# Optimization experiments

Measured on AMD Instinct MI355X. Metric: run time of the kernel, lower is better.

## Reference

```python
import jax, jax.numpy as jnp
import numpy as np

E, NH, NL, NP = 256, 8, 4, 4
D = E // NH
SPATIAL_SHAPES = np.array([[100, 134], [50, 67], [25, 34], [13, 17]], dtype=np.int64)
B = 2


def setup_inputs() -> dict:
    key = jax.random.key(0)
    ks = jax.random.split(key, 12)
    Lin = int((SPATIAL_SHAPES[:, 0] * SPATIAL_SHAPES[:, 1]).sum())
    Lq = Lin
    s = 0.02
    return {
        'query': jax.random.normal(ks[0], (Lq, B, E), jnp.float32),
        'value': jax.random.normal(ks[1], (Lin, B, E), jnp.float32),
        'reference_points': jax.random.uniform(ks[2], (B, Lq, NL, 2), jnp.float32),
        'spatial_shapes': SPATIAL_SHAPES,
        'W_value': jax.random.normal(ks[3], (E, E), jnp.float32) * s,
        'b_value': jnp.zeros((E,), jnp.float32),
        'W_offset': jax.random.normal(ks[4], (E, NH * NL * NP * 2), jnp.float32) * s,
        'b_offset': jax.random.normal(ks[5], (NH * NL * NP * 2,), jnp.float32) * 0.5,
        'W_attn': jax.random.normal(ks[6], (E, NH * NL * NP), jnp.float32) * s,
        'b_attn': jnp.zeros((NH * NL * NP,), jnp.float32),
        'W_out': jax.random.normal(ks[7], (E, E), jnp.float32) * s,
        'b_out': jnp.zeros((E,), jnp.float32),
    }


def _ms_deform_attn(value, spatial_shapes, sampling_locations, attention_weights):
    # value: (B, Lin, NH, D); sampling_locations: (B, Lq, NH, NL, NP, 2) in [0,1]
    # attention_weights: (B, Lq, NH, NL, NP)
    b, _, nh, d = value.shape
    lq = sampling_locations.shape[1]
    npnt = sampling_locations.shape[4]
    shapes = np.asarray(spatial_shapes)
    out = jnp.zeros((b, nh, lq, d), value.dtype)
    start = 0
    for l in range(shapes.shape[0]):
        H, W = int(shapes[l, 0]), int(shapes[l, 1])
        vl = value[:, start:start + H * W].transpose(0, 2, 1, 3)  # (B, NH, H*W, D)
        loc = sampling_locations[:, :, :, l].transpose(0, 2, 1, 3, 4)  # (B, NH, Lq, P, 2)
        # grid_sample align_corners=False convention (matches CUDA kernel)
        x = loc[..., 0] * W - 0.5
        y = loc[..., 1] * H - 0.5
        x0 = jnp.floor(x)
        y0 = jnp.floor(y)
        dx = x - x0
        dy = y - y0
        x0i = x0.astype(jnp.int32)
        y0i = y0.astype(jnp.int32)
        acc = jnp.zeros((b, nh, lq, npnt, d), value.dtype)
        corners = [
            (x0i, y0i, (1.0 - dx) * (1.0 - dy)),
            (x0i + 1, y0i, dx * (1.0 - dy)),
            (x0i, y0i + 1, (1.0 - dx) * dy),
            (x0i + 1, y0i + 1, dx * dy),
        ]
        for xi, yi, w in corners:
            valid = ((xi >= 0) & (xi < W) & (yi >= 0) & (yi < H)).astype(value.dtype)
            idx = jnp.clip(yi, 0, W - 1 if False else H - 1) * 0  # placeholder removed below
            idx = jnp.clip(yi, 0, H - 1) * W + jnp.clip(xi, 0, W - 1)  # (B, NH, Lq, P)
            g = jnp.take_along_axis(vl, idx.reshape(b, nh, -1)[..., None], axis=2)
            g = g.reshape(b, nh, lq, npnt, d)
            acc = acc + g * (w * valid)[..., None]
        awl = attention_weights[:, :, :, l].transpose(0, 2, 1, 3)  # (B, NH, Lq, P)
        out = out + jnp.einsum('bhqpd,bhqp->bhqd', acc, awl)
        start += H * W
    return out.transpose(0, 2, 1, 3).reshape(b, lq, nh * d)  # (B, Lq, E)


def reference(query, value, reference_points, spatial_shapes,
              W_value, b_value, W_offset, b_offset, W_attn, b_attn, W_out, b_out):
    q = query.transpose(1, 0, 2)   # (B, Lq, E)
    v = value.transpose(1, 0, 2)   # (B, Lin, E)
    b, lq, _ = q.shape
    lin = v.shape[1]
    v = (v @ W_value + b_value).reshape(b, lin, NH, D)
    offsets = (q @ W_offset + b_offset).reshape(b, lq, NH, NL, NP, 2)
    attn = (q @ W_attn + b_attn).reshape(b, lq, NH, NL, NP)
    attn = jax.nn.softmax(attn, axis=-1)  # softmax over points (as in source)
    shapes_f = jnp.asarray(np.asarray(spatial_shapes), jnp.float32)
    offset_normalizer = jnp.stack([shapes_f[:, 1], shapes_f[:, 0]], -1)  # (NL, 2) = (w, h)
    loc = reference_points[:, :, None, :, None, :] + offsets / offset_normalizer[None, None, None, :, None, :]
    out = _ms_deform_attn(v, spatial_shapes, loc, attn)  # (B, Lq, E)
    out = out @ W_out + b_out
    return out.transpose(1, 0, 2)  # (Lq, B, E)
```

## Files before the change

kernel.cpp:

```cpp
#include <hip/hip_runtime.h>
#include <math.h>

#define LQ    17821
#define MROWS 35642
#define KD    256

typedef __attribute__((ext_vector_type(8))) short bf16x8;
typedef __attribute__((ext_vector_type(4))) float f32x4;

__device__ __forceinline__ short f2bf(float f) {
  union { float f; unsigned u; } c; c.f = f;
  unsigned u = c.u;
  return (short)((u + 0x7fffu + ((u >> 16) & 1u)) >> 16);
}
__device__ __forceinline__ float bf2f(short s) {
  union { unsigned u; float f; } c;
  c.u = ((unsigned)(unsigned short)s) << 16;
  return c.f;
}

__global__ __launch_bounds__(256) void cvt_bf16(
    const float* __restrict__ src, short* __restrict__ dst, int n)
{
  int i = (blockIdx.x * 256 + threadIdx.x) * 4;
  if (i < n) {
    float4 v = *(const float4*)(src + i);
    short4 o;
    o.x = f2bf(v.x); o.y = f2bf(v.y); o.z = f2bf(v.z); o.w = f2bf(v.w);
    *(short4*)(dst + i) = o;
  }
}

__global__ __launch_bounds__(256) void wtrans_all(
    const float* __restrict__ Wv, const float* __restrict__ Woff,
    const float* __restrict__ Wat, const float* __restrict__ Wout,
    short* __restrict__ wT)
{
  int sel = blockIdx.y;
  const float* W = sel == 0 ? Wv : sel == 1 ? Woff : sel == 2 ? Wat : Wout;
  short* Wt = wT + (sel == 0 ? 0 : sel == 1 ? 65536 : sel == 2 ? 131072 : 163840);
  int N = (sel == 2) ? 128 : 256;
  int idx = blockIdx.x * 256 + threadIdx.x;
  if (idx < N * 256) {
    int n = idx >> 8, k = idx & 255;
    Wt[idx] = f2bf(W[k * N + n]);
  }
}

template<bool OUT_BF16>
__global__ __launch_bounds__(256) void gemm_bf16(
    const short* __restrict__ A, const short* __restrict__ Bt,
    const float* __restrict__ bias, void* __restrict__ Cout,
    int M, int N)
{
  __shared__ short As[128 * 40];
  __shared__ short Bs[128 * 40];

  const int tid = threadIdx.x;
  const int bm = blockIdx.x * 128;
  const int bn = blockIdx.y * 128;
  const int wave = tid >> 6;
  const int lane = tid & 63;
  const int wm = (wave & 1) * 64;
  const int wn = (wave >> 1) * 64;
  const int ln = lane & 15;
  const int lk = (lane >> 4) * 8;

  f32x4 acc[4][4];
#pragma unroll
  for (int i = 0; i < 4; ++i)
#pragma unroll
    for (int j = 0; j < 4; ++j) acc[i][j] = (f32x4){0.f, 0.f, 0.f, 0.f};

  const int r0 = tid >> 2,         s0 = (tid & 3) * 8;
  const int r1 = (tid + 256) >> 2, s1 = ((tid + 256) & 3) * 8;
  const size_t arow0 = (size_t)min(bm + r0, M - 1) * KD;
  const size_t arow1 = (size_t)min(bm + r1, M - 1) * KD;
  const size_t brow0 = (size_t)(bn + r0) * KD;
  const size_t brow1 = (size_t)(bn + r1) * KD;

  for (int k0 = 0; k0 < KD; k0 += 32) {
    bf16x8 a0 = *(const bf16x8*)(A + arow0 + k0 + s0);
    bf16x8 a1 = *(const bf16x8*)(A + arow1 + k0 + s1);
    bf16x8 b0 = *(const bf16x8*)(Bt + brow0 + k0 + s0);
    bf16x8 b1 = *(const bf16x8*)(Bt + brow1 + k0 + s1);
    __syncthreads();
    *(bf16x8*)&As[r0 * 40 + s0] = a0;
    *(bf16x8*)&As[r1 * 40 + s1] = a1;
    *(bf16x8*)&Bs[r0 * 40 + s0] = b0;
    *(bf16x8*)&Bs[r1 * 40 + s1] = b1;
    __syncthreads();

    bf16x8 af[4], bfr[4];
#pragma unroll
    for (int i = 0; i < 4; ++i)
      af[i] = *(const bf16x8*)&As[(wm + i * 16 + ln) * 40 + lk];
#pragma unroll
    for (int j = 0; j < 4; ++j)
      bfr[j] = *(const bf16x8*)&Bs[(wn + j * 16 + ln) * 40 + lk];
#pragma unroll
    for (int i = 0; i < 4; ++i)
#pragma unroll
      for (int j = 0; j < 4; ++j)
        acc[i][j] = __builtin_amdgcn_mfma_f32_16x16x32_bf16(af[i], bfr[j], acc[i][j], 0, 0, 0);
  }

#pragma unroll
  for (int j = 0; j < 4; ++j) {
    const int col = bn + wn + j * 16 + ln;
    const float bb = bias[col];
#pragma unroll
    for (int i = 0; i < 4; ++i) {
      const int row0 = bm + wm + i * 16 + (lane >> 4) * 4;
#pragma unroll
      for (int r = 0; r < 4; ++r) {
        const int row = row0 + r;
        if (row < M) {
          float v = acc[i][j][r] + bb;
          if (OUT_BF16)
            ((short*)Cout)[(size_t)row * N + col] = f2bf(v);
          else
            ((float*)Cout)[(size_t)row * N + col] = v;
        }
      }
    }
  }
}

__global__ __launch_bounds__(256) void msda_sample(
    const short* __restrict__ vproj, const float* __restrict__ offs,
    const float* __restrict__ attn, const float* __restrict__ refp,
    short* __restrict__ out)
{
  static constexpr int LVL_H[4] = {100, 50, 25, 13};
  static constexpr int LVL_W[4] = {134, 67, 34, 17};
  static constexpr int LVL_S[4] = {0, 13400, 16750, 17600};

  __shared__ int4   s_off[4 * 8 * 17];
  __shared__ float4 s_w[4 * 8 * 17];

  const int tid = threadIdx.x;
  const int m0 = blockIdx.x * 4;

#pragma unroll
  for (int it = 0; it < 2; ++it) {
    int w = tid + it * 256;
    int mr = w >> 7;
    int rest = w & 127;
    int h = rest >> 4;
    int lp = rest & 15;
    int l = lp >> 2;
    int p = lp & 3;
    int m = m0 + mr;
    if (m < MROWS) {
      int b = m & 1, q = m >> 1;
      const int Hl = LVL_H[l], Wl = LVL_W[l], Sl = LVL_S[l];
      const float fW = (float)Wl, fH = (float)Hl;

      const float* aRow = attn + (size_t)m * 128 + h * 16 + l * 4;
      float a0 = aRow[0], a1 = aRow[1], a2 = aRow[2], a3 = aRow[3];
      float mx = fmaxf(fmaxf(a0, a1), fmaxf(a2, a3));
      a0 = __expf(a0 - mx); a1 = __expf(a1 - mx);
      a2 = __expf(a2 - mx); a3 = __expf(a3 - mx);
      float sel = (p == 0) ? a0 : (p == 1) ? a1 : (p == 2) ? a2 : a3;
      float aw = sel / (a0 + a1 + a2 + a3);

      const float* oPtr = offs + (size_t)m * 256 + h * 32 + l * 8 + p * 2;
      float ox = oPtr[0], oy = oPtr[1];
      const float* rPtr = refp + ((size_t)b * LQ + q) * 8 + l * 2;
      float rx = rPtr[0], ry = rPtr[1];

      float x = (rx + ox / fW) * fW - 0.5f;
      float y = (ry + oy / fH) * fH - 0.5f;
      float x0f = floorf(x), y0f = floorf(y);
      float dx = x - x0f, dy = y - y0f;
      int x0 = (int)x0f, y0 = (int)y0f;
      int x1 = x0 + 1, y1 = y0 + 1;

      float w00 = (1.f - dx) * (1.f - dy) * aw;
      float w10 = dx * (1.f - dy) * aw;
      float w01 = (1.f - dx) * dy * aw;
      float w11 = dx * dy * aw;

      bool vx0 = (x0 >= 0) & (x0 < Wl);
      bool vx1 = (x1 >= 0) & (x1 < Wl);
      bool vy0 = (y0 >= 0) & (y0 < Hl);
      bool vy1 = (y1 >= 0) & (y1 < Hl);
      int cx0 = min(max(x0, 0), Wl - 1);
      int cx1 = min(max(x1, 0), Wl - 1);
      int cy0 = min(max(y0, 0), Hl - 1);
      int cy1 = min(max(y1, 0), Hl - 1);

      int r0 = Sl + cy0 * Wl;
      int r1 = Sl + cy1 * Wl;
      int e = (mr * 8 + h) * 17 + lp;
      s_off[e] = make_int4(((r0 + cx0) * 2 + b) << 8,
                           ((r0 + cx1) * 2 + b) << 8,
                           ((r1 + cx0) * 2 + b) << 8,
                           ((r1 + cx1) * 2 + b) << 8);
      s_w[e] = make_float4((vy0 & vx0) ? w00 : 0.f,
                           (vy0 & vx1) ? w10 : 0.f,
                           (vy1 & vx0) ? w01 : 0.f,
                           (vy1 & vx1) ? w11 : 0.f);
    }
  }
  __syncthreads();

  const int mr = tid >> 6;
  const int t = tid & 63;
  const int h = t >> 3;
  const int dq = t & 7;
  const int m = m0 + mr;
  if (m >= MROWS) return;

  const int laneOff = h * 32 + dq * 4;
  const int ebase = (mr * 8 + h) * 17;
  float4 acc = make_float4(0.f, 0.f, 0.f, 0.f);

#pragma unroll 4
  for (int lp = 0; lp < 16; ++lp) {
    int4 off = s_off[ebase + lp];
    float4 wv = s_w[ebase + lp];
    short4 u00 = *(const short4*)(vproj + off.x + laneOff);
    short4 u10 = *(const short4*)(vproj + off.y + laneOff);
    short4 u01 = *(const short4*)(vproj + off.z + laneOff);
    short4 u11 = *(const short4*)(vproj + off.w + laneOff);
    acc.x = fmaf(wv.x, bf2f(u00.x), acc.x);
    acc.y = fmaf(wv.x, bf2f(u00.y), acc.y);
    acc.z = fmaf(wv.x, bf2f(u00.z), acc.z);
    acc.w = fmaf(wv.x, bf2f(u00.w), acc.w);
    acc.x = fmaf(wv.y, bf2f(u10.x), acc.x);
    acc.y = fmaf(wv.y, bf2f(u10.y), acc.y);
    acc.z = fmaf(wv.y, bf2f(u10.z), acc.z);
    acc.w = fmaf(wv.y, bf2f(u10.w), acc.w);
    acc.x = fmaf(wv.z, bf2f(u01.x), acc.x);
    acc.y = fmaf(wv.z, bf2f(u01.y), acc.y);
    acc.z = fmaf(wv.z, bf2f(u01.z), acc.z);
    acc.w = fmaf(wv.z, bf2f(u01.w), acc.w);
    acc.x = fmaf(wv.w, bf2f(u11.x), acc.x);
    acc.y = fmaf(wv.w, bf2f(u11.y), acc.y);
    acc.z = fmaf(wv.w, bf2f(u11.z), acc.z);
    acc.w = fmaf(wv.w, bf2f(u11.w), acc.w);
  }

  short4 o;
  o.x = f2bf(acc.x); o.y = f2bf(acc.y); o.z = f2bf(acc.z); o.w = f2bf(acc.w);
  *(short4*)(out + (size_t)m * 256 + laneOff) = o;
}

extern "C" void kernel_launch(void* const* d_in, const int* in_sizes, int n_in,
                              void* d_out, int out_size, void* d_ws, size_t ws_size,
                              hipStream_t stream)
{
  const float* query = (const float*)d_in[0];
  const float* value = (const float*)d_in[1];
  const float* refp  = (const float*)d_in[2];
  const float* Wv   = (const float*)d_in[4];
  const float* bv   = (const float*)d_in[5];
  const float* Woff = (const float*)d_in[6];
  const float* boff = (const float*)d_in[7];
  const float* Wat  = (const float*)d_in[8];
  const float* bat  = (const float*)d_in[9];
  const float* Wout = (const float*)d_in[10];
  const float* bout = (const float*)d_in[11];
  float* out = (float*)d_out;

  const size_t NELT = (size_t)MROWS * 256;
  short* query_bf = (short*)d_ws;
  short* value_bf = query_bf + NELT;
  short* vproj    = value_bf + NELT;
  short* wT       = vproj + NELT;
  float* offsb    = (float*)(wT + 229376);
  float* attnb    = offsb + NELT;
  short* accb     = value_bf;

  dim3 blk(256, 1, 1);
  int gm = (MROWS + 127) / 128;

  cvt_bf16<<<dim3(8911), blk, 0, stream>>>(query, query_bf, MROWS * 256);
  cvt_bf16<<<dim3(8911), blk, 0, stream>>>(value, value_bf, MROWS * 256);
  wtrans_all<<<dim3(256, 4), blk, 0, stream>>>(Wv, Woff, Wat, Wout, wT);

  gemm_bf16<true ><<<dim3(gm, 2), blk, 0, stream>>>(value_bf, wT,          bv,   vproj, MROWS, 256);
  gemm_bf16<false><<<dim3(gm, 2), blk, 0, stream>>>(query_bf, wT + 65536,  boff, offsb, MROWS, 256);
  gemm_bf16<false><<<dim3(gm, 1), blk, 0, stream>>>(query_bf, wT + 131072, bat,  attnb, MROWS, 128);

  msda_sample<<<dim3((MROWS + 3) / 4), blk, 0, stream>>>(vproj, offsb, attnb, refp, accb);

  gemm_bf16<false><<<dim3(gm, 2), blk, 0, stream>>>(accb, wT + 163840, bout, out, MROWS, 256);
}
```

Baseline: 308.0 us.

## Fuse fp32-to-bf16 conversion into GEMMs and merge offset/attn projections

Removes the separate conversion kernels by having the GEMM load fp32 activations and convert them to bf16 while staging into shared memory. The offset and attention-logit projections become a single N=384 GEMM with a concatenated bias, so the query is read once, and the sampler reads both from one interleaved buffer. The sampling kernel now handles 8 queries per block with 8-element bf16 vector gathers per thread. This cuts kernel launches and intermediate buffer traffic, at the cost of the GEMM reading wider fp32 A rows and doing the conversion inside its loop.

After: 302.6 us. About the same (-1.8%).

```diff
diff --git a/kernel.cpp b/kernel.cpp
--- a/kernel.cpp
+++ b/kernel.cpp
@@ -19,37 +19,30 @@
   return c.f;
 }
 
-__global__ __launch_bounds__(256) void cvt_bf16(
-    const float* __restrict__ src, short* __restrict__ dst, int n)
-{
-  int i = (blockIdx.x * 256 + threadIdx.x) * 4;
-  if (i < n) {
-    float4 v = *(const float4*)(src + i);
-    short4 o;
-    o.x = f2bf(v.x); o.y = f2bf(v.y); o.z = f2bf(v.z); o.w = f2bf(v.w);
-    *(short4*)(dst + i) = o;
-  }
-}
-
 __global__ __launch_bounds__(256) void wtrans_all(
     const float* __restrict__ Wv, const float* __restrict__ Woff,
     const float* __restrict__ Wat, const float* __restrict__ Wout,
-    short* __restrict__ wT)
+    const float* __restrict__ boff, const float* __restrict__ bat,
+    short* __restrict__ wT, float* __restrict__ fbias)
 {
   int sel = blockIdx.y;
+  int idx = blockIdx.x * 256 + threadIdx.x;
+  if (sel == 4) {
+    if (idx < 384) fbias[idx] = (idx < 256) ? boff[idx] : bat[idx - 256];
+    return;
+  }
   const float* W = sel == 0 ? Wv : sel == 1 ? Woff : sel == 2 ? Wat : Wout;
   short* Wt = wT + (sel == 0 ? 0 : sel == 1 ? 65536 : sel == 2 ? 131072 : 163840);
   int N = (sel == 2) ? 128 : 256;
-  int idx = blockIdx.x * 256 + threadIdx.x;
   if (idx < N * 256) {
     int n = idx >> 8, k = idx & 255;
     Wt[idx] = f2bf(W[k * N + n]);
   }
 }
 
-template<bool OUT_BF16>
+template<bool A_F32, bool OUT_BF16>
 __global__ __launch_bounds__(256) void gemm_bf16(
-    const short* __restrict__ A, const short* __restrict__ Bt,
+    const void* __restrict__ Araw, const short* __restrict__ Bt,
     const float* __restrict__ bias, void* __restrict__ Cout,
     int M, int N)
 {
@@ -72,23 +65,38 @@
 #pragma unroll
     for (int j = 0; j < 4; ++j) acc[i][j] = (f32x4){0.f, 0.f, 0.f, 0.f};
 
-  const int r0 = tid >> 2,         s0 = (tid & 3) * 8;
-  const int r1 = (tid + 256) >> 2, s1 = ((tid + 256) & 3) * 8;
+  const int r0 = tid >> 2,  s0 = (tid & 3) * 8;
+  const int r1 = r0 + 64;
   const size_t arow0 = (size_t)min(bm + r0, M - 1) * KD;
   const size_t arow1 = (size_t)min(bm + r1, M - 1) * KD;
   const size_t brow0 = (size_t)(bn + r0) * KD;
   const size_t brow1 = (size_t)(bn + r1) * KD;
 
+  const short* Ab = (const short*)Araw;
+  const float* Af = (const float*)Araw;
+
   for (int k0 = 0; k0 < KD; k0 += 32) {
-    bf16x8 a0 = *(const bf16x8*)(A + arow0 + k0 + s0);
-    bf16x8 a1 = *(const bf16x8*)(A + arow1 + k0 + s1);
+    bf16x8 a0, a1;
+    if (A_F32) {
+      float4 p0 = *(const float4*)(Af + arow0 + k0 + s0);
+      float4 p1 = *(const float4*)(Af + arow0 + k0 + s0 + 4);
+      float4 p2 = *(const float4*)(Af + arow1 + k0 + s0);
+      float4 p3 = *(const float4*)(Af + arow1 + k0 + s0 + 4);
+      a0[0] = f2bf(p0.x); a0[1] = f2bf(p0.y); a0[2] = f2bf(p0.z); a0[3] = f2bf(p0.w);
+      a0[4] = f2bf(p1.x); a0[5] = f2bf(p1.y); a0[6] = f2bf(p1.z); a0[7] = f2bf(p1.w);
+      a1[0] = f2bf(p2.x); a1[1] = f2bf(p2.y); a1[2] = f2bf(p2.z); a1[3] = f2bf(p2.w);
+      a1[4] = f2bf(p3.x); a1[5] = f2bf(p3.y); a1[6] = f2bf(p3.z); a1[7] = f2bf(p3.w);
+    } else {
+      a0 = *(const bf16x8*)(Ab + arow0 + k0 + s0);
+      a1 = *(const bf16x8*)(Ab + arow1 + k0 + s0);
+    }
     bf16x8 b0 = *(const bf16x8*)(Bt + brow0 + k0 + s0);
-    bf16x8 b1 = *(const bf16x8*)(Bt + brow1 + k0 + s1);
+    bf16x8 b1 = *(const bf16x8*)(Bt + brow1 + k0 + s0);
     __syncthreads();
     *(bf16x8*)&As[r0 * 40 + s0] = a0;
-    *(bf16x8*)&As[r1 * 40 + s1] = a1;
+    *(bf16x8*)&As[r1 * 40 + s0] = a1;
     *(bf16x8*)&Bs[r0 * 40 + s0] = b0;
-    *(bf16x8*)&Bs[r1 * 40 + s1] = b1;
+    *(bf16x8*)&Bs[r1 * 40 + s0] = b1;
     __syncthreads();
 
     bf16x8 af[4], bfr[4];
@@ -128,22 +136,21 @@
 }
 
 __global__ __launch_bounds__(256) void msda_sample(
-    const short* __restrict__ vproj, const float* __restrict__ offs,
-    const float* __restrict__ attn, const float* __restrict__ refp,
-    short* __restrict__ out)
+    const short* __restrict__ vproj, const float* __restrict__ oa,
+    const float* __restrict__ refp, short* __restrict__ out)
 {
   static constexpr int LVL_H[4] = {100, 50, 25, 13};
   static constexpr int LVL_W[4] = {134, 67, 34, 17};
   static constexpr int LVL_S[4] = {0, 13400, 16750, 17600};
 
-  __shared__ int4   s_off[4 * 8 * 17];
-  __shared__ float4 s_w[4 * 8 * 17];
+  __shared__ int4   s_off[8 * 8 * 17];
+  __shared__ float4 s_w[8 * 8 * 17];
 
   const int tid = threadIdx.x;
-  const int m0 = blockIdx.x * 4;
-
-#pragma unroll
-  for (int it = 0; it < 2; ++it) {
+  const int m0 = blockIdx.x * 8;
+
+#pragma unroll
+  for (int it = 0; it < 4; ++it) {
     int w = tid + it * 256;
     int mr = w >> 7;
     int rest = w & 127;
@@ -157,15 +164,15 @@
       const int Hl = LVL_H[l], Wl = LVL_W[l], Sl = LVL_S[l];
       const float fW = (float)Wl, fH = (float)Hl;
 
-      const float* aRow = attn + (size_t)m * 128 + h * 16 + l * 4;
-      float a0 = aRow[0], a1 = aRow[1], a2 = aRow[2], a3 = aRow[3];
+      float4 av = *(const float4*)(oa + (size_t)m * 384 + 256 + h * 16 + l * 4);
+      float a0 = av.x, a1 = av.y, a2 = av.z, a3 = av.w;
       float mx = fmaxf(fmaxf(a0, a1), fmaxf(a2, a3));
       a0 = __expf(a0 - mx); a1 = __expf(a1 - mx);
       a2 = __expf(a2 - mx); a3 = __expf(a3 - mx);
       float sel = (p == 0) ? a0 : (p == 1) ? a1 : (p == 2) ? a2 : a3;
       float aw = sel / (a0 + a1 + a2 + a3);
 
-      const float* oPtr = offs + (size_t)m * 256 + h * 32 + l * 8 + p * 2;
+      const float* oPtr = oa + (size_t)m * 384 + h * 32 + l * 8 + p * 2;
       float ox = oPtr[0], oy = oPtr[1];
       const float* rPtr = refp + ((size_t)b * LQ + q) * 8 + l * 2;
       float rx = rPtr[0], ry = rPtr[1];
@@ -206,46 +213,40 @@
   }
   __syncthreads();
 
-  const int mr = tid >> 6;
-  const int t = tid & 63;
-  const int h = t >> 3;
-  const int dq = t & 7;
+  const int mr = tid >> 5;
+  const int t = tid & 31;
+  const int h = t >> 2;
+  const int dq = t & 3;
   const int m = m0 + mr;
   if (m >= MROWS) return;
 
-  const int laneOff = h * 32 + dq * 4;
+  const int laneOff = h * 32 + dq * 8;
   const int ebase = (mr * 8 + h) * 17;
-  float4 acc = make_float4(0.f, 0.f, 0.f, 0.f);
+  float acc[8];
+#pragma unroll
+  for (int e = 0; e < 8; ++e) acc[e] = 0.f;
 
 #pragma unroll 4
   for (int lp = 0; lp < 16; ++lp) {
     int4 off = s_off[ebase + lp];
     float4 wv = s_w[ebase + lp];
-    short4 u00 = *(const short4*)(vproj + off.x + laneOff);
-    short4 u10 = *(const short4*)(vproj + off.y + laneOff);
-    short4 u01 = *(const short4*)(vproj + off.z + laneOff);
-    short4 u11 = *(const short4*)(vproj + off.w + laneOff);
-    acc.x = fmaf(wv.x, bf2f(u00.x), acc.x);
-    acc.y = fmaf(wv.x, bf2f(u00.y), acc.y);
-    acc.z = fmaf(wv.x, bf2f(u00.z), acc.z);
-    acc.w = fmaf(wv.x, bf2f(u00.w), acc.w);
-    acc.x = fmaf(wv.y, bf2f(u10.x), acc.x);
-    acc.y = fmaf(wv.y, bf2f(u10.y), acc.y);
-    acc.z = fmaf(wv.y, bf2f(u10.z), acc.z);
-    acc.w = fmaf(wv.y, bf2f(u10.w), acc.w);
-    acc.x = fmaf(wv.z, bf2f(u01.x), acc.x);
-    acc.y = fmaf(wv.z, bf2f(u01.y), acc.y);
-    acc.z = fmaf(wv.z, bf2f(u01.z), acc.z);
-    acc.w = fmaf(wv.z, bf2f(u01.w), acc.w);
-    acc.x = fmaf(wv.w, bf2f(u11.x), acc.x);
-    acc.y = fmaf(wv.w, bf2f(u11.y), acc.y);
-    acc.z = fmaf(wv.w, bf2f(u11.z), acc.z);
-    acc.w = fmaf(wv.w, bf2f(u11.w), acc.w);
-  }
-
-  short4 o;
-  o.x = f2bf(acc.x); o.y = f2bf(acc.y); o.z = f2bf(acc.z); o.w = f2bf(acc.w);
-  *(short4*)(out + (size_t)m * 256 + laneOff) = o;
+    bf16x8 u00 = *(const bf16x8*)(vproj + off.x + laneOff);
+    bf16x8 u10 = *(const bf16x8*)(vproj + off.y + laneOff);
+    bf16x8 u01 = *(const bf16x8*)(vproj + off.z + laneOff);
+    bf16x8 u11 = *(const bf16x8*)(vproj + off.w + laneOff);
+#pragma unroll
+    for (int e = 0; e < 8; ++e) {
+      acc[e] = fmaf(wv.x, bf2f(u00[e]), acc[e]);
+      acc[e] = fmaf(wv.y, bf2f(u10[e]), acc[e]);
+      acc[e] = fmaf(wv.z, bf2f(u01[e]), acc[e]);
+      acc[e] = fmaf(wv.w, bf2f(u11[e]), acc[e]);
+    }
+  }
+
+  bf16x8 o;
+#pragma unroll
+  for (int e = 0; e < 8; ++e) o[e] = f2bf(acc[e]);
+  *(bf16x8*)(out + (size_t)m * 256 + laneOff) = o;
 }
 
 extern "C" void kernel_launch(void* const* d_in, const int* in_sizes, int n_in,
@@ -266,26 +267,21 @@
   float* out = (float*)d_out;
 
   const size_t NELT = (size_t)MROWS * 256;
-  short* query_bf = (short*)d_ws;
-  short* value_bf = query_bf + NELT;
-  short* vproj    = value_bf + NELT;
-  short* wT       = vproj + NELT;
-  float* offsb    = (float*)(wT + 229376);
-  float* attnb    = offsb + NELT;
-  short* accb     = value_bf;
+  short* wT    = (short*)d_ws;
+  float* fbias = (float*)(wT + 229376);
+  short* vproj = (short*)(fbias + 384);
+  short* accb  = vproj + NELT;
+  float* oa    = (float*)(accb + NELT);
 
   dim3 blk(256, 1, 1);
   int gm = (MROWS + 127) / 128;
 
-  cvt_bf16<<<dim3(8911), blk, 0, stream>>>(query, query_bf, MROWS * 256);
-  cvt_bf16<<<dim3(8911), blk, 0, stream>>>(value, value_bf, MROWS * 256);
-  wtrans_all<<<dim3(256, 4), blk, 0, stream>>>(Wv, Woff, Wat, Wout, wT);
-
-  gemm_bf16<true ><<<dim3(gm, 2), blk, 0, stream>>>(value_bf, wT,          bv,   vproj, MROWS, 256);
-  gemm_bf16<false><<<dim3(gm, 2), blk, 0, stream>>>(query_bf, wT + 65536,  boff, offsb, MROWS, 256);
-  gemm_bf16<false><<<dim3(gm, 1), blk, 0, stream>>>(query_bf, wT + 131072, bat,  attnb, MROWS, 128);
-
-  msda_sample<<<dim3((MROWS + 3) / 4), blk, 0, stream>>>(vproj, offsb, attnb, refp, accb);
-
-  gemm_bf16<false><<<dim3(gm, 2), blk, 0, stream>>>(accb, wT + 163840, bout, out, MROWS, 256);
-}
+  wtrans_all<<<dim3(256, 5), blk, 0, stream>>>(Wv, Woff, Wat, Wout, boff, bat, wT, fbias);
+
+  gemm_bf16<true,  true ><<<dim3(gm, 2), blk, 0, stream>>>(value, wT,         bv,    vproj, MROWS, 256);
+  gemm_bf16<true,  false><<<dim3(gm, 3), blk, 0, stream>>>(query, wT + 65536, fbias, oa,    MROWS, 384);
+
+  msda_sample<<<dim3((MROWS + 7) / 8), blk, 0, stream>>>(vproj, oa, refp, accb);
+
+  gemm_bf16<false, false><<<dim3(gm, 2), blk, 0, stream>>>(accb, wT + 163840, bout, out, MROWS, 256);
+}
```
